# Optimization experiments

Measured on AMD Instinct MI355X. Metric: run time of the kernel, lower is better.

Reference implementation:

```python
import jax, jax.numpy as jnp
from jax import lax
import numpy as np

N, T, U = 8, 300, 60
E_ENC, E_DEC, NHID, VOCAB, BLANK = 320, 320, 512, 128, 0


def setup_inputs() -> dict:
    key = jax.random.key(0)
    ks = jax.random.split(key, 6)
    enc_state = jax.random.normal(ks[0], (N, T, E_ENC), jnp.float32)
    dec_state = jax.random.normal(ks[1], (N, U + 1, E_DEC), jnp.float32)
    targets = jax.random.randint(ks[2], (N, U), 1, VOCAB, jnp.int32)  # non-blank labels
    inputs_len = jnp.full((N,), T, jnp.int32)
    targets_len = jnp.full((N,), U, jnp.int32)
    W_joint = jax.random.normal(ks[3], (E_ENC + E_DEC, NHID), jnp.float32) * (1.0 / np.sqrt(E_ENC + E_DEC))
    b_joint = jnp.zeros((NHID,), jnp.float32)
    W_out = jax.random.normal(ks[4], (NHID, VOCAB), jnp.float32) * (1.0 / np.sqrt(NHID))
    b_out = jnp.zeros((VOCAB,), jnp.float32)
    return dict(enc_state=enc_state, dec_state=dec_state, targets=targets,
                inputs_len=inputs_len, targets_len=targets_len,
                W_joint=W_joint, b_joint=b_joint, W_out=W_out, b_out=b_out)


def _joint_log_probs(enc, dec, Wj, bj, Wo, bo):
    # Original: broadcast enc [N,T,1,Ee] + dec [N,1,U1,Ed], concat, Linear, Tanh, Linear, log_softmax.
    # Splitting W_joint over the concat axis is exactly equivalent and avoids the [N,T,U1,Ee+Ed] tensor.
    Ee = enc.shape[-1]
    h = (jnp.einsum('nte,eh->nth', enc, Wj[:Ee])[:, :, None, :]
         + jnp.einsum('nue,eh->nuh', dec, Wj[Ee:])[:, None, :, :]
         + bj)                                              # [N,T,U1,NHID]
    logits = jnp.einsum('ntuh,hv->ntuv', jnp.tanh(h), Wo) + bo  # [N,T,U1,V]
    return jax.nn.log_softmax(logits, axis=-1)


def _rnnt_loss(logp, targets, inputs_len, targets_len, blank):
    # Forward (alpha) DP over the T x (U+1) lattice, vectorized over batch.
    Nb, Tt, U1, V = logp.shape
    blank_lp = logp[..., blank]                                        # [N,T,U1]
    emit_lp = jnp.take_along_axis(logp[:, :, :U1 - 1, :],
                                  targets[:, None, :, None], axis=-1)[..., 0]  # [N,T,U]
    # Row t=0: alpha[0,u] = sum_{u'<u} emit[0,u'].
    a0 = jnp.concatenate([jnp.zeros((Nb, 1), logp.dtype),
                          jnp.cumsum(emit_lp[:, 0, :], axis=1)], axis=1)       # [N,U1]

    def row_step(prev, xs):
        blank_tm1, emit_t = xs                      # [N,U1], [N,U]
        base = prev + blank_tm1                     # path arriving from (t-1,u) via blank

        def u_step(carry, xs_u):
            b_u, e_u = xs_u                         # [N], [N]
            v = jnp.logaddexp(b_u, carry + e_u)     # blank-from-below vs emit-from-left
            return v, v

        _, rest = lax.scan(u_step, base[:, 0], (base[:, 1:].T, emit_t.T))      # [U,N]
        row = jnp.concatenate([base[:, :1], rest.T], axis=1)                   # [N,U1]
        return row, row

    _, rows = lax.scan(row_step, a0,
                       (jnp.swapaxes(blank_lp[:, :-1], 0, 1),
                        jnp.swapaxes(emit_lp[:, 1:], 0, 1)))                   # [T-1,N,U1]
    alpha = jnp.concatenate([a0[:, None, :], jnp.swapaxes(rows, 0, 1)], axis=1)  # [N,T,U1]

    ti = (inputs_len - 1).astype(jnp.int32)
    ui = targets_len.astype(jnp.int32)
    n = jnp.arange(Nb)
    log_p = alpha[n, ti, ui] + blank_lp[n, ti, ui]  # final blank transition
    return -log_p


def reference(enc_state, dec_state, targets, inputs_len, targets_len,
              W_joint, b_joint, W_out, b_out):
    logp = _joint_log_probs(enc_state, dec_state, W_joint, b_joint, W_out, b_out)
    loss = _rnnt_loss(logp, targets, inputs_len, targets_len, BLANK)
    return loss.mean()
```

## Files before the change

### kernel.cpp

```cpp
#include <hip/hip_runtime.h>
#include <hip/hip_bf16.h>
#include <hip/hip_fp16.h>

#define N_   8
#define T_   300
#define U_   60
#define U1_  61
#define EENC 320
#define NHID 512
#define VOC  128
#define SKROWS 384
#define INV_LN2 1.4426950408889634f
#define LN2 0.6931471805599453f
#define SCALE2 2.8853900817779268f

typedef __attribute__((ext_vector_type(8))) short bf16x8;
typedef __attribute__((ext_vector_type(4))) float f32x4;

__device__ __forceinline__ unsigned short f2bf(float f) {
    unsigned int u = __float_as_uint(f);
    u += 0x7fff + ((u >> 16) & 1);
    return (unsigned short)(u >> 16);
}

__device__ __forceinline__ float lae2(float x, float y) {
    float m = fmaxf(x, y);
    float d = fminf(fabsf(x - y), 1e30f);
    return m + log2f(1.f + exp2f(-d));
}

__device__ __forceinline__ unsigned gload4(const void* p) {
    unsigned v;
    asm volatile("global_load_dword %0, %1, off" : "=v"(v) : "v"(p) : "memory");
    return v;
}

__global__ __launch_bounds__(256) void convert_w(
    const float* __restrict__ Wj, const float* __restrict__ Wo,
    unsigned short* __restrict__ WjT, unsigned short* __restrict__ WoT2,
    float* __restrict__ bosum)
{
    __shared__ float tile[32][33];
    int bid = blockIdx.x;
    const float* S; unsigned short* D; int k0, c0, K, C; bool isWo;
    if (bid < 160) { S = Wj; D = WjT; K = 320; C = 512; k0 = (bid >> 4) * 32; c0 = (bid & 15) * 32; isWo = false; }
    else { bid -= 160; S = Wo; D = WoT2; K = 512; C = 128; k0 = (bid >> 2) * 32; c0 = (bid & 3) * 32; isWo = true; }
    const int tx = threadIdx.x & 31, ty = threadIdx.x >> 5;
    float part = 0.f;
    #pragma unroll
    for (int i = 0; i < 32; i += 8) {
        float v = S[(k0 + ty + i) * C + c0 + tx];
        tile[ty + i][tx] = v;
        part += v;
    }
    __syncthreads();
    const float mulf = isWo ? -2.f : 1.f;
    #pragma unroll
    for (int i = 0; i < 32; i += 8)
        D[(c0 + ty + i) * K + k0 + tx] = f2bf(mulf * tile[tx][ty + i]);
    if (isWo) atomicAdd(&bosum[c0 + tx], part);
}

__global__ __launch_bounds__(256) void proj_mfma(
    const float* __restrict__ Xe, const float* __restrict__ Xd,
    const unsigned short* __restrict__ BT,
    const float* __restrict__ bj,
    float* __restrict__ Ce, float* __restrict__ Cd)
{
    __shared__ short lA[64 * 64];
    __shared__ short lB[128 * 64];
    int bid = blockIdx.x;
    const float* X; float* Cp; const float* bias; int R;
    if (bid < 152) { X = Xe; Cp = Ce; bias = nullptr; R = N_ * T_; }
    else { bid -= 152; X = Xd; Cp = Cd; bias = bj; R = N_ * U1_; }
    const int tid = threadIdx.x, lane = tid & 63, wave = tid >> 6;
    const int rb = bid >> 2, cb = bid & 3;
    const int rh = wave & 1, ch = wave >> 1;
    const int sr = tid >> 3, sg = tid & 7;
    const int frow = lane & 15, fg = lane >> 4, quad = lane >> 4;

    f32x4 acc[2][4];
    f32x4 z = {0.f, 0.f, 0.f, 0.f};
    #pragma unroll
    for (int a = 0; a < 2; ++a)
        #pragma unroll
        for (int b = 0; b < 4; ++b) acc[a][b] = z;

    for (int s = 0; s < 5; ++s) {
        __syncthreads();
        #pragma unroll
        for (int p = 0; p < 2; ++p) {
            int row = sr + p * 32;
            int grow = rb * 64 + row; if (grow >= R) grow = R - 1;
            const float* xp = X + grow * EENC + s * 64 + sg * 8;
            float4 x0 = *(const float4*)xp, x1 = *(const float4*)(xp + 4);
            bf16x8 va;
            va[0] = (short)f2bf(x0.x); va[1] = (short)f2bf(x0.y);
            va[2] = (short)f2bf(x0.z); va[3] = (short)f2bf(x0.w);
            va[4] = (short)f2bf(x1.x); va[5] = (short)f2bf(x1.y);
            va[6] = (short)f2bf(x1.z); va[7] = (short)f2bf(x1.w);
            *(bf16x8*)&lA[row * 64 + ((sg ^ (row & 7)) << 3)] = va;
        }
        #pragma unroll
        for (int p = 0; p < 4; ++p) {
            int col = sr + p * 32;
            bf16x8 vb = *(const bf16x8*)(BT + (cb * 128 + col) * EENC + s * 64 + sg * 8);
            *(bf16x8*)&lB[col * 64 + ((sg ^ (col & 7)) << 3)] = vb;
        }
        __syncthreads();
        #pragma unroll
        for (int ks = 0; ks < 2; ++ks) {
            int g = fg + ks * 4;
            bf16x8 af[2], bf[4];
            #pragma unroll
            for (int rt = 0; rt < 2; ++rt) {
                int row = rh * 32 + rt * 16 + frow;
                af[rt] = *(const bf16x8*)&lA[row * 64 + ((g ^ (row & 7)) << 3)];
            }
            #pragma unroll
            for (int c = 0; c < 4; ++c) {
                int col = ch * 64 + c * 16 + frow;
                bf[c] = *(const bf16x8*)&lB[col * 64 + ((g ^ (col & 7)) << 3)];
            }
            #pragma unroll
            for (int rt = 0; rt < 2; ++rt)
                #pragma unroll
                for (int c = 0; c < 4; ++c)
                    acc[rt][c] = __builtin_amdgcn_mfma_f32_16x16x32_bf16(af[rt], bf[c], acc[rt][c], 0, 0, 0);
        }
    }
    #pragma unroll
    for (int rt = 0; rt < 2; ++rt) {
        int grow0 = rb * 64 + rh * 32 + rt * 16 + quad * 4;
        #pragma unroll
        for (int c = 0; c < 4; ++c) {
            int col = cb * 128 + ch * 64 + c * 16 + frow;
            float b = bias ? bias[col] : 0.f;
            #pragma unroll
            for (int r = 0; r < 4; ++r) {
                int gr = grow0 + r;
                if (gr < R) Cp[gr * NHID + col] = (acc[rt][c][r] + b) * SCALE2;
            }
        }
    }
}

__global__ __launch_bounds__(512, 4) void joint_mfma(
    const float* __restrict__ encp,
    const float* __restrict__ decp,
    const unsigned short* __restrict__ WoT2,
    const float* __restrict__ bo, const float* __restrict__ bosum,
    const int* __restrict__ targets,
    unsigned short* __restrict__ Zs)
{
    __shared__ short lA[256 * 64];
    __shared__ short lB[128 * 64];
    __shared__ float bo_s[VOC];
    __shared__ int   lab_s[U_];

    const int tid = threadIdx.x, lane = tid & 63, wave = tid >> 6;
    const int nt0 = 4 * blockIdx.x, n = nt0 / T_;
    const int t0 = nt0 - n * T_;
    if (tid < VOC) bo_s[tid] = bo[tid] + bosum[tid];
    else if (tid < VOC + U_) lab_s[tid - VOC] = targets[n * U_ + (tid - VOC)];

    const int frow = lane & 15, quad = lane >> 4;
    const int sg = tid & 7, sr = tid >> 3;

    f32x4 acc[2][8];
    f32x4 z = {0.f, 0.f, 0.f, 0.f};
    #pragma unroll
    for (int rt = 0; rt < 2; ++rt)
        #pragma unroll
        for (int c = 0; c < 8; ++c) acc[rt][c] = z;

    const int ua = min(sr, U_);
    const float* dbase = decp + (size_t)(n * U1_ + ua) * NHID + sg * 8;
    const float* ebase = encp + (size_t)nt0 * NHID + sg * 8;

    for (int s = 0; s < 8; ++s) {
        __syncthreads();
        #pragma unroll
        for (int p = 0; p < 2; ++p) {
            int col = sr + p * 64;
            bf16x8 vb = *(const bf16x8*)(WoT2 + col * NHID + s * 64 + sg * 8);
            *(bf16x8*)&lB[col * 64 + ((sg ^ (col & 7)) << 3)] = vb;
        }
        const float* dp = dbase + s * 64;
        float4 d0 = *(const float4*)dp, d1 = *(const float4*)(dp + 4);
        #pragma unroll
        for (int p = 0; p < 4; ++p) {
            const float* ep = ebase + (size_t)p * NHID + s * 64;
            float4 e0 = *(const float4*)ep, e1 = *(const float4*)(ep + 4);
            float s0 = __builtin_amdgcn_rcpf(__builtin_amdgcn_exp2f(e0.x + d0.x) + 1.f);
            float s1 = __builtin_amdgcn_rcpf(__builtin_amdgcn_exp2f(e0.y + d0.y) + 1.f);
            float s2 = __builtin_amdgcn_rcpf(__builtin_amdgcn_exp2f(e0.z + d0.z) + 1.f);
            float s3 = __builtin_amdgcn_rcpf(__builtin_amdgcn_exp2f(e0.w + d0.w) + 1.f);
            float s4 = __builtin_amdgcn_rcpf(__builtin_amdgcn_exp2f(e1.x + d1.x) + 1.f);
            float s5 = __builtin_amdgcn_rcpf(__builtin_amdgcn_exp2f(e1.y + d1.y) + 1.f);
            float s6 = __builtin_amdgcn_rcpf(__builtin_amdgcn_exp2f(e1.z + d1.z) + 1.f);
            float s7 = __builtin_amdgcn_rcpf(__builtin_amdgcn_exp2f(e1.w + d1.w) + 1.f);
            unsigned b0 = __float_as_uint(s0) + 0x8000u, b1 = __float_as_uint(s1) + 0x8000u;
            unsigned b2 = __float_as_uint(s2) + 0x8000u, b3 = __float_as_uint(s3) + 0x8000u;
            unsigned b4 = __float_as_uint(s4) + 0x8000u, b5 = __float_as_uint(s5) + 0x8000u;
            unsigned b6 = __float_as_uint(s6) + 0x8000u, b7 = __float_as_uint(s7) + 0x8000u;
            union { unsigned u4[4]; bf16x8 v; } va;
            va.u4[0] = __builtin_amdgcn_perm(b1, b0, 0x07060302);
            va.u4[1] = __builtin_amdgcn_perm(b3, b2, 0x07060302);
            va.u4[2] = __builtin_amdgcn_perm(b5, b4, 0x07060302);
            va.u4[3] = __builtin_amdgcn_perm(b7, b6, 0x07060302);
            int row = sr + p * 64;
            *(bf16x8*)&lA[row * 64 + ((sg ^ (row & 7)) << 3)] = va.v;
        }
        __syncthreads();
        #pragma unroll
        for (int ks = 0; ks < 2; ++ks) {
            const int g = ks * 4 + quad;
            bf16x8 af[2];
            #pragma unroll
            for (int rt = 0; rt < 2; ++rt) {
                int ar = wave * 32 + rt * 16 + frow;
                af[rt] = *(const bf16x8*)&lA[ar * 64 + ((g ^ (ar & 7)) << 3)];
            }
            #pragma unroll
            for (int c = 0; c < 8; ++c) {
                int col = c * 16 + frow;
                const bf16x8 bfr = *(const bf16x8*)&lB[col * 64 + ((g ^ (col & 7)) << 3)];
                acc[0][c] = __builtin_amdgcn_mfma_f32_16x16x32_bf16(af[0], bfr, acc[0][c], 0, 0, 0);
                acc[1][c] = __builtin_amdgcn_mfma_f32_16x16x32_bf16(af[1], bfr, acc[1][c], 0, 0, 0);
            }
        }
    }

    #pragma unroll
    for (int rt = 0; rt < 2; ++rt) {
        #pragma unroll
        for (int c = 0; c < 8; ++c) {
            float b = bo_s[c * 16 + frow];
            #pragma unroll
            for (int r = 0; r < 4; ++r) acc[rt][c][r] += b;
        }
        float mx[4], sm[4];
        #pragma unroll
        for (int r = 0; r < 4; ++r) {
            float m = acc[rt][0][r];
            #pragma unroll
            for (int c = 1; c < 8; ++c) m = fmaxf(m, acc[rt][c][r]);
            mx[r] = m;
        }
        #pragma unroll
        for (int off = 1; off < 16; off <<= 1)
            #pragma unroll
            for (int r = 0; r < 4; ++r) mx[r] = fmaxf(mx[r], __shfl_xor(mx[r], off));
        #pragma unroll
        for (int r = 0; r < 4; ++r) {
            float ss = 0.f;
            #pragma unroll
            for (int c = 0; c < 8; ++c) ss += __expf(acc[rt][c][r] - mx[r]);
            sm[r] = ss;
        }
        #pragma unroll
        for (int off = 1; off < 16; off <<= 1)
            #pragma unroll
            for (int r = 0; r < 4; ++r) sm[r] += __shfl_xor(sm[r], off);

        #pragma unroll
        for (int r = 0; r < 4; ++r) {
            float lse = mx[r] + __logf(sm[r]);
            int row = wave * 32 + rt * 16 + quad * 4 + r;
            int urow = row & 63, ntl = row >> 6;
            size_t rowz = (size_t)(n * SKROWS + t0 + ntl + urow + 1) * 64;
            if (urow < U1_ && frow == 0) {
                __half hh = __float2half_rn((acc[rt][0][r] - lse) * INV_LN2);
                Zs[(rowz + urow) * 2] = __half_as_ushort(hh);
            }
            if (urow < U_) {
                int lab = lab_s[urow];
                if (frow == (lab & 15)) {
                    int cw = lab >> 4;
                    float pick = acc[rt][0][r];
                    #pragma unroll
                    for (int c = 1; c < 8; ++c) if (c == cw) pick = acc[rt][c][r];
                    __half hh = __float2half_rn((pick - lse) * INV_LN2);
                    Zs[(rowz + urow + 1) * 2 + 1] = __half_as_ushort(hh);
                }
            }
        }
    }
}

__global__ __launch_bounds__(512) void dp_kernel(
    const unsigned* __restrict__ Z,
    const int* __restrict__ inputs_len, const int* __restrict__ targets_len,
    float* __restrict__ out)
{
    __shared__ float losses[N_];
    const int tid = threadIdx.x;
    const int n = tid >> 6;
    const int u = tid & 63;
    const bool u_is0 = (u == 0);

    const unsigned len_t = (unsigned)inputs_len[n];
    const int ui = targets_len[n];
    const int ti = (int)len_t - 1;

    const char* Zn = (const char*)(Z + (size_t)n * SKROWS * 64) + u * 4;

    float a = u_is0 ? 0.f : -1e30f;

    unsigned zq[16];
    #pragma unroll
    for (int j = 0; j < 16; ++j) zq[j] = gload4(Zn + (size_t)(1 + j) * 256);

    for (int d0 = 1; d0 < 361; d0 += 16) {
        const char* pn = Zn + (size_t)(d0 + 16) * 256;
        #pragma unroll
        for (int j = 0; j < 16; ++j) {
            const int d = d0 + j;
            asm volatile("s_waitcnt vmcnt(15)");
            asm volatile("" : "+v"(zq[j]));
            unsigned zv = zq[j];
            zq[j] = gload4(pn + (size_t)j * 256);
            union { unsigned u32; __half2 h2; } cv; cv.u32 = zv;
            float2 w = __half22float2(cv.h2);
            float av = __shfl_up(a, 1);
            float b  = a + w.x;
            float e  = av + (u_is0 ? -1e30f : w.y);
            float nn = lae2(b, e);
            a = ((unsigned)(d - u) < len_t) ? nn : a;
        }
    }

    if (u == ui) {
        const unsigned* Zb = Z + (size_t)n * SKROWS * 64;
        unsigned wf = Zb[(size_t)(ti + ui + 1) * 64 + ui];
        union { unsigned u32; __half2 h2; } cf; cf.u32 = wf;
        float blf = __half22float2(cf.h2).x;
        losses[n] = -(a + blf) * LN2;
    }
    __syncthreads();
    if (tid == 0) {
        float s = 0.f;
        #pragma unroll
        for (int i = 0; i < N_; ++i) s += losses[i];
        out[0] = s * (1.0f / N_);
    }
}

extern "C" void kernel_launch(void* const* d_in, const int* in_sizes, int n_in,
                              void* d_out, int out_size, void* d_ws, size_t ws_size,
                              hipStream_t stream)
{
    const float* enc         = (const float*)d_in[0];
    const float* dec         = (const float*)d_in[1];
    const int*   targets     = (const int*)d_in[2];
    const int*   inputs_len  = (const int*)d_in[3];
    const int*   targets_len = (const int*)d_in[4];
    const float* Wj          = (const float*)d_in[5];
    const float* bj          = (const float*)d_in[6];
    const float* Wo          = (const float*)d_in[7];
    const float* bo          = (const float*)d_in[8];
    float* out = (float*)d_out;

    char* ws = (char*)d_ws;
    float*          encp  = (float*)(ws + 0);
    float*          decp  = (float*)(ws + 4915200);
    unsigned*       Z     = (unsigned*)(ws + 5914624);
    unsigned short* WjT   = (unsigned short*)(ws + 6701056);
    unsigned short* WoT2  = (unsigned short*)(ws + 7028736);
    float*          bosum = (float*)(ws + 7159872);

    hipMemsetAsync(bosum, 0, VOC * sizeof(float), stream);
    convert_w<<<224, 256, 0, stream>>>(Wj, Wo, WjT, WoT2, bosum);
    proj_mfma<<<184, 256, 0, stream>>>(enc, dec, WjT, bj, encp, decp);
    joint_mfma<<<600, 512, 0, stream>>>(encp, decp, WoT2, bo, bosum, targets, (unsigned short*)Z);
    dp_kernel<<<1, 512, 0, stream>>>(Z, inputs_len, targets_len, out);
}
```

Measured before the change: 188.3 us.

## Shrink joint tile to one timestep per block and prefetch next K-slice into registers

Each joint block now covers a single (n,t) row of 64 u-values with 256 threads instead of four timesteps with 512, and the grid grows from 600 to 2400 blocks. Global loads for the next K-slice of enc, dec and WoT2 are issued into registers before the MFMA loop so their latency overlaps compute, and s_setprio raises priority around the MFMA section. The trade-off is that each WoT2 slice is reloaded per timestep, giving four times the weight traffic and less reuse in exchange for more parallelism and better latency hiding.

```diff
diff --git a/kernel.cpp b/kernel.cpp
--- a/kernel.cpp
+++ b/kernel.cpp
@@ -145,7 +145,30 @@
     }
 }
 
-__global__ __launch_bounds__(512, 4) void joint_mfma(
+__device__ __forceinline__ void sigstore(short* lAp, float4 ee0, float4 ee1,
+                                         float4 dd0, float4 dd1, int row, int sg)
+{
+    float s0 = __builtin_amdgcn_rcpf(__builtin_amdgcn_exp2f(ee0.x + dd0.x) + 1.f);
+    float s1 = __builtin_amdgcn_rcpf(__builtin_amdgcn_exp2f(ee0.y + dd0.y) + 1.f);
+    float s2 = __builtin_amdgcn_rcpf(__builtin_amdgcn_exp2f(ee0.z + dd0.z) + 1.f);
+    float s3 = __builtin_amdgcn_rcpf(__builtin_amdgcn_exp2f(ee0.w + dd0.w) + 1.f);
+    float s4 = __builtin_amdgcn_rcpf(__builtin_amdgcn_exp2f(ee1.x + dd1.x) + 1.f);
+    float s5 = __builtin_amdgcn_rcpf(__builtin_amdgcn_exp2f(ee1.y + dd1.y) + 1.f);
+    float s6 = __builtin_amdgcn_rcpf(__builtin_amdgcn_exp2f(ee1.z + dd1.z) + 1.f);
+    float s7 = __builtin_amdgcn_rcpf(__builtin_amdgcn_exp2f(ee1.w + dd1.w) + 1.f);
+    unsigned b0 = __float_as_uint(s0) + 0x8000u, b1 = __float_as_uint(s1) + 0x8000u;
+    unsigned b2 = __float_as_uint(s2) + 0x8000u, b3 = __float_as_uint(s3) + 0x8000u;
+    unsigned b4 = __float_as_uint(s4) + 0x8000u, b5 = __float_as_uint(s5) + 0x8000u;
+    unsigned b6 = __float_as_uint(s6) + 0x8000u, b7 = __float_as_uint(s7) + 0x8000u;
+    union { unsigned u4[4]; bf16x8 v; } va;
+    va.u4[0] = __builtin_amdgcn_perm(b1, b0, 0x07060302);
+    va.u4[1] = __builtin_amdgcn_perm(b3, b2, 0x07060302);
+    va.u4[2] = __builtin_amdgcn_perm(b5, b4, 0x07060302);
+    va.u4[3] = __builtin_amdgcn_perm(b7, b6, 0x07060302);
+    *(bf16x8*)&lAp[row * 64 + ((sg ^ (row & 7)) << 3)] = va.v;
+}
+
+__global__ __launch_bounds__(256, 4) void joint_mfma(
     const float* __restrict__ encp,
     const float* __restrict__ decp,
     const unsigned short* __restrict__ WoT2,
@@ -153,137 +176,125 @@
     const int* __restrict__ targets,
     unsigned short* __restrict__ Zs)
 {
-    __shared__ short lA[256 * 64];
+    __shared__ short lA[64 * 64];
     __shared__ short lB[128 * 64];
     __shared__ float bo_s[VOC];
     __shared__ int   lab_s[U_];
 
     const int tid = threadIdx.x, lane = tid & 63, wave = tid >> 6;
-    const int nt0 = 4 * blockIdx.x, n = nt0 / T_;
-    const int t0 = nt0 - n * T_;
+    const int nt = blockIdx.x;
+    const int n = nt / T_, t0 = nt - n * T_;
     if (tid < VOC) bo_s[tid] = bo[tid] + bosum[tid];
     else if (tid < VOC + U_) lab_s[tid - VOC] = targets[n * U_ + (tid - VOC)];
 
     const int frow = lane & 15, quad = lane >> 4;
     const int sg = tid & 7, sr = tid >> 3;
 
-    f32x4 acc[2][8];
+    f32x4 acc[8];
     f32x4 z = {0.f, 0.f, 0.f, 0.f};
     #pragma unroll
-    for (int rt = 0; rt < 2; ++rt)
-        #pragma unroll
-        for (int c = 0; c < 8; ++c) acc[rt][c] = z;
-
-    const int ua = min(sr, U_);
-    const float* dbase = decp + (size_t)(n * U1_ + ua) * NHID + sg * 8;
-    const float* ebase = encp + (size_t)nt0 * NHID + sg * 8;
+    for (int c = 0; c < 8; ++c) acc[c] = z;
+
+    const int ua0 = min(sr, U_);
+    const int ua1 = min(sr + 32, U_);
+    const float* dbase0 = decp + (size_t)(n * U1_ + ua0) * NHID + sg * 8;
+    const float* dbase1 = decp + (size_t)(n * U1_ + ua1) * NHID + sg * 8;
+    const float* ebase  = encp + (size_t)nt * NHID + sg * 8;
+    const unsigned short* wbase = WoT2 + sg * 8;
+
+    float4 e0, e1, d00, d01, d10, d11;
+    bf16x8 vb0, vb1, vb2, vb3;
+    e0  = *(const float4*)ebase;        e1  = *(const float4*)(ebase + 4);
+    d00 = *(const float4*)dbase0;       d01 = *(const float4*)(dbase0 + 4);
+    d10 = *(const float4*)dbase1;       d11 = *(const float4*)(dbase1 + 4);
+    vb0 = *(const bf16x8*)(wbase + (size_t)(sr +  0) * NHID);
+    vb1 = *(const bf16x8*)(wbase + (size_t)(sr + 32) * NHID);
+    vb2 = *(const bf16x8*)(wbase + (size_t)(sr + 64) * NHID);
+    vb3 = *(const bf16x8*)(wbase + (size_t)(sr + 96) * NHID);
 
     for (int s = 0; s < 8; ++s) {
         __syncthreads();
-        #pragma unroll
-        for (int p = 0; p < 2; ++p) {
-            int col = sr + p * 64;
-            bf16x8 vb = *(const bf16x8*)(WoT2 + col * NHID + s * 64 + sg * 8);
-            *(bf16x8*)&lB[col * 64 + ((sg ^ (col & 7)) << 3)] = vb;
-        }
-        const float* dp = dbase + s * 64;
-        float4 d0 = *(const float4*)dp, d1 = *(const float4*)(dp + 4);
-        #pragma unroll
-        for (int p = 0; p < 4; ++p) {
-            const float* ep = ebase + (size_t)p * NHID + s * 64;
-            float4 e0 = *(const float4*)ep, e1 = *(const float4*)(ep + 4);
-            float s0 = __builtin_amdgcn_rcpf(__builtin_amdgcn_exp2f(e0.x + d0.x) + 1.f);
-            float s1 = __builtin_amdgcn_rcpf(__builtin_amdgcn_exp2f(e0.y + d0.y) + 1.f);
-            float s2 = __builtin_amdgcn_rcpf(__builtin_amdgcn_exp2f(e0.z + d0.z) + 1.f);
-            float s3 = __builtin_amdgcn_rcpf(__builtin_amdgcn_exp2f(e0.w + d0.w) + 1.f);
-            float s4 = __builtin_amdgcn_rcpf(__builtin_amdgcn_exp2f(e1.x + d1.x) + 1.f);
-            float s5 = __builtin_amdgcn_rcpf(__builtin_amdgcn_exp2f(e1.y + d1.y) + 1.f);
-            float s6 = __builtin_amdgcn_rcpf(__builtin_amdgcn_exp2f(e1.z + d1.z) + 1.f);
-            float s7 = __builtin_amdgcn_rcpf(__builtin_amdgcn_exp2f(e1.w + d1.w) + 1.f);
-            unsigned b0 = __float_as_uint(s0) + 0x8000u, b1 = __float_as_uint(s1) + 0x8000u;
-            unsigned b2 = __float_as_uint(s2) + 0x8000u, b3 = __float_as_uint(s3) + 0x8000u;
-            unsigned b4 = __float_as_uint(s4) + 0x8000u, b5 = __float_as_uint(s5) + 0x8000u;
-            unsigned b6 = __float_as_uint(s6) + 0x8000u, b7 = __float_as_uint(s7) + 0x8000u;
-            union { unsigned u4[4]; bf16x8 v; } va;
-            va.u4[0] = __builtin_amdgcn_perm(b1, b0, 0x07060302);
-            va.u4[1] = __builtin_amdgcn_perm(b3, b2, 0x07060302);
-            va.u4[2] = __builtin_amdgcn_perm(b5, b4, 0x07060302);
-            va.u4[3] = __builtin_amdgcn_perm(b7, b6, 0x07060302);
-            int row = sr + p * 64;
-            *(bf16x8*)&lA[row * 64 + ((sg ^ (row & 7)) << 3)] = va.v;
-        }
+        { int col = sr;      *(bf16x8*)&lB[col * 64 + ((sg ^ (col & 7)) << 3)] = vb0; }
+        { int col = sr + 32; *(bf16x8*)&lB[col * 64 + ((sg ^ (col & 7)) << 3)] = vb1; }
+        { int col = sr + 64; *(bf16x8*)&lB[col * 64 + ((sg ^ (col & 7)) << 3)] = vb2; }
+        { int col = sr + 96; *(bf16x8*)&lB[col * 64 + ((sg ^ (col & 7)) << 3)] = vb3; }
+        sigstore(lA, e0, e1, d00, d01, sr,      sg);
+        sigstore(lA, e0, e1, d10, d11, sr + 32, sg);
         __syncthreads();
+        if (s < 7) {
+            const int o = (s + 1) * 64;
+            e0  = *(const float4*)(ebase + o);      e1  = *(const float4*)(ebase + o + 4);
+            d00 = *(const float4*)(dbase0 + o);     d01 = *(const float4*)(dbase0 + o + 4);
+            d10 = *(const float4*)(dbase1 + o);     d11 = *(const float4*)(dbase1 + o + 4);
+            vb0 = *(const bf16x8*)(wbase + (size_t)(sr +  0) * NHID + o);
+            vb1 = *(const bf16x8*)(wbase + (size_t)(sr + 32) * NHID + o);
+            vb2 = *(const bf16x8*)(wbase + (size_t)(sr + 64) * NHID + o);
+            vb3 = *(const bf16x8*)(wbase + (size_t)(sr + 96) * NHID + o);
+        }
+        __builtin_amdgcn_s_setprio(1);
         #pragma unroll
         for (int ks = 0; ks < 2; ++ks) {
             const int g = ks * 4 + quad;
-            bf16x8 af[2];
-            #pragma unroll
-            for (int rt = 0; rt < 2; ++rt) {
-                int ar = wave * 32 + rt * 16 + frow;
-                af[rt] = *(const bf16x8*)&lA[ar * 64 + ((g ^ (ar & 7)) << 3)];
-            }
+            int ar = wave * 16 + frow;
+            bf16x8 af = *(const bf16x8*)&lA[ar * 64 + ((g ^ (ar & 7)) << 3)];
             #pragma unroll
             for (int c = 0; c < 8; ++c) {
                 int col = c * 16 + frow;
                 const bf16x8 bfr = *(const bf16x8*)&lB[col * 64 + ((g ^ (col & 7)) << 3)];
-                acc[0][c] = __builtin_amdgcn_mfma_f32_16x16x32_bf16(af[0], bfr, acc[0][c], 0, 0, 0);
-                acc[1][c] = __builtin_amdgcn_mfma_f32_16x16x32_bf16(af[1], bfr, acc[1][c], 0, 0, 0);
-            }
-        }
-    }
-
-    #pragma unroll
-    for (int rt = 0; rt < 2; ++rt) {
-        #pragma unroll
-        for (int c = 0; c < 8; ++c) {
-            float b = bo_s[c * 16 + frow];
-            #pragma unroll
-            for (int r = 0; r < 4; ++r) acc[rt][c][r] += b;
-        }
-        float mx[4], sm[4];
-        #pragma unroll
-        for (int r = 0; r < 4; ++r) {
-            float m = acc[rt][0][r];
-            #pragma unroll
-            for (int c = 1; c < 8; ++c) m = fmaxf(m, acc[rt][c][r]);
-            mx[r] = m;
-        }
-        #pragma unroll
-        for (int off = 1; off < 16; off <<= 1)
-            #pragma unroll
-            for (int r = 0; r < 4; ++r) mx[r] = fmaxf(mx[r], __shfl_xor(mx[r], off));
-        #pragma unroll
-        for (int r = 0; r < 4; ++r) {
-            float ss = 0.f;
-            #pragma unroll
-            for (int c = 0; c < 8; ++c) ss += __expf(acc[rt][c][r] - mx[r]);
-            sm[r] = ss;
-        }
-        #pragma unroll
-        for (int off = 1; off < 16; off <<= 1)
-            #pragma unroll
-            for (int r = 0; r < 4; ++r) sm[r] += __shfl_xor(sm[r], off);
-
-        #pragma unroll
-        for (int r = 0; r < 4; ++r) {
-            float lse = mx[r] + __logf(sm[r]);
-            int row = wave * 32 + rt * 16 + quad * 4 + r;
-            int urow = row & 63, ntl = row >> 6;
-            size_t rowz = (size_t)(n * SKROWS + t0 + ntl + urow + 1) * 64;
-            if (urow < U1_ && frow == 0) {
-                __half hh = __float2half_rn((acc[rt][0][r] - lse) * INV_LN2);
-                Zs[(rowz + urow) * 2] = __half_as_ushort(hh);
-            }
-            if (urow < U_) {
-                int lab = lab_s[urow];
-                if (frow == (lab & 15)) {
-                    int cw = lab >> 4;
-                    float pick = acc[rt][0][r];
-                    #pragma unroll
-                    for (int c = 1; c < 8; ++c) if (c == cw) pick = acc[rt][c][r];
-                    __half hh = __float2half_rn((pick - lse) * INV_LN2);
-                    Zs[(rowz + urow + 1) * 2 + 1] = __half_as_ushort(hh);
-                }
+                acc[c] = __builtin_amdgcn_mfma_f32_16x16x32_bf16(af, bfr, acc[c], 0, 0, 0);
+            }
+        }
+        __builtin_amdgcn_s_setprio(0);
+    }
+
+    #pragma unroll
+    for (int c = 0; c < 8; ++c) {
+        float b = bo_s[c * 16 + frow];
+        #pragma unroll
+        for (int r = 0; r < 4; ++r) acc[c][r] += b;
+    }
+    float mx[4], sm[4];
+    #pragma unroll
+    for (int r = 0; r < 4; ++r) {
+        float m = acc[0][r];
+        #pragma unroll
+        for (int c = 1; c < 8; ++c) m = fmaxf(m, acc[c][r]);
+        mx[r] = m;
+    }
+    #pragma unroll
+    for (int off = 1; off < 16; off <<= 1)
+        #pragma unroll
+        for (int r = 0; r < 4; ++r) mx[r] = fmaxf(mx[r], __shfl_xor(mx[r], off));
+    #pragma unroll
+    for (int r = 0; r < 4; ++r) {
+        float ss = 0.f;
+        #pragma unroll
+        for (int c = 0; c < 8; ++c) ss += __expf(acc[c][r] - mx[r]);
+        sm[r] = ss;
+    }
+    #pragma unroll
+    for (int off = 1; off < 16; off <<= 1)
+        #pragma unroll
+        for (int r = 0; r < 4; ++r) sm[r] += __shfl_xor(sm[r], off);
+
+    #pragma unroll
+    for (int r = 0; r < 4; ++r) {
+        float lse = mx[r] + __logf(sm[r]);
+        int urow = wave * 16 + quad * 4 + r;
+        size_t rowz = (size_t)(n * SKROWS + t0 + urow + 1) * 64;
+        if (urow < U1_ && frow == 0) {
+            __half hh = __float2half_rn((acc[0][r] - lse) * INV_LN2);
+            Zs[(rowz + urow) * 2] = __half_as_ushort(hh);
+        }
+        if (urow < U_) {
+            int lab = lab_s[urow];
+            if (frow == (lab & 15)) {
+                int cw = lab >> 4;
+                float pick = acc[0][r];
+                #pragma unroll
+                for (int c = 1; c < 8; ++c) if (c == cw) pick = acc[c][r];
+                __half hh = __float2half_rn((pick - lse) * INV_LN2);
+                Zs[(rowz + urow + 1) * 2 + 1] = __half_as_ushort(hh);
             }
         }
     }
@@ -373,6 +384,6 @@
     hipMemsetAsync(bosum, 0, VOC * sizeof(float), stream);
     convert_w<<<224, 256, 0, stream>>>(Wj, Wo, WjT, WoT2, bosum);
     proj_mfma<<<184, 256, 0, stream>>>(enc, dec, WjT, bj, encp, decp);
-    joint_mfma<<<600, 512, 0, stream>>>(encp, decp, WoT2, bo, bosum, targets, (unsigned short*)Z);
+    joint_mfma<<<2400, 256, 0, stream>>>(encp, decp, WoT2, bo, bosum, targets, (unsigned short*)Z);
     dp_kernel<<<1, 512, 0, stream>>>(Z, inputs_len, targets_len, out);
 }
```

Result: faster. 184.5 us (-2.0%).
